# Kernel optimization log

Measured on AMD Instinct MI355X. Metric: run time of the kernel, lower is better.

Reference implementation:

```python
import jax, jax.numpy as jnp
import numpy as np

B, C, Hf, Wf, HM, P = 64, 2048, 16, 16, 256, 10  # P = num_parts, NP = graph nodes
NP = P - 1
EPS = 1e-5  # BatchNorm eps

def bn_eval(x, g, b, rm, rv):
    return (x - rm) * jax.lax.rsqrt(rv + EPS) * g + b

def setup_inputs() -> dict:
    key = jax.random.key(0)
    ks = jax.random.split(key, 6)
    return {
        "x_global": jax.random.normal(ks[0], (B, C, Hf, Wf), jnp.float32),
        "x_gcn": jax.random.normal(ks[1], (B, C, Hf, Wf), jnp.float32),
        "mask": jax.random.randint(ks[2], (B, 1, HM, HM), 0, P, jnp.int32),
        "adj": jax.random.uniform(ks[3], (B, NP, NP), jnp.float32),
        "W1": jax.random.normal(ks[4], (C, C), jnp.float32) * 0.02,
        "b1": jnp.zeros((C,), jnp.float32),
        "g1": jnp.ones((NP * C,), jnp.float32), "be1": jnp.zeros((NP * C,), jnp.float32),
        "rm1": jnp.zeros((NP * C,), jnp.float32), "rv1": jnp.ones((NP * C,), jnp.float32),
        "W2": jax.random.normal(ks[5], (C, C), jnp.float32) * 0.02,
        "b2": jnp.zeros((C,), jnp.float32),
        "g2": jnp.ones((NP * C,), jnp.float32), "be2": jnp.zeros((NP * C,), jnp.float32),
        "rm2": jnp.zeros((NP * C,), jnp.float32), "rv2": jnp.ones((NP * C,), jnp.float32),
        "gb_g": jnp.ones((C,), jnp.float32), "gb_b": jnp.zeros((C,), jnp.float32),
        "gb_rm": jnp.zeros((C,), jnp.float32), "gb_rv": jnp.ones((C,), jnp.float32),
        "gn_g": jnp.ones((C,), jnp.float32), "gn_b": jnp.zeros((C,), jnp.float32),
        "gn_rm": jnp.zeros((C,), jnp.float32), "gn_rv": jnp.ones((C,), jnp.float32),
    }

def gc_layer(x, adj, Wt, bias, g, be, rm, rv):
    # GraphConvolution: matmul -> bmm(adj) -> bias -> BN over flattened (B, NP*C)
    s = jnp.einsum('bpc,cd->bpd', x, Wt)
    o = jnp.einsum('bpq,bqd->bpd', adj, s) + bias
    flat = o.reshape(o.shape[0], -1)
    return bn_eval(flat, g, be, rm, rv).reshape(o.shape)

def reference(x_global, x_gcn, mask, adj, W1, b1, g1, be1, rm1, rv1,
              W2, b2, g2, be2, rm2, rv2, gb_g, gb_b, gb_rm, gb_rv,
              gn_g, gn_b, gn_rm, gn_rv):
    # --- global branch: GAP + bottleneck BN (eval) ---
    feat_global = x_global.mean(axis=(2, 3))                      # (B, C)
    bnfeat_global = bn_eval(feat_global, gb_g, gb_b, gb_rm, gb_rv)

    # --- nearest-neighbor downsample of mask to feature-map size ---
    stride = HM // Hf
    mr = mask[:, 0, ::stride, ::stride]                           # (B, h, w)

    # one-hot part masks for classes 1..P-1: (B, h, w, NP)
    onehot = (mr[..., None] == jnp.arange(1, P)).astype(jnp.float32)
    counts = onehot.sum(axis=(1, 2))                              # (B, NP)

    # deterministic part dropout: drop the first present part per image
    drop = jnp.argmax(counts > 0, axis=1) + 1                     # (B,)
    keep = (mr != drop[:, None, None]).astype(jnp.float32)        # (B, h, w)
    x_self = x_gcn * keep[:, None, :, :]

    # segment mean pooling per part: (B, NP, C)
    denom = (counts + 1e-8)[..., None]
    mask_feat = jnp.einsum('bchw,bhwp->bpc', x_gcn, onehot) / denom
    self_feat = jnp.einsum('bchw,bhwp->bpc', x_self, onehot) / denom

    def gcn(x):
        x1 = jax.nn.relu(gc_layer(x, adj, W1, b1, g1, be1, rm1, rv1))
        x2 = jax.nn.relu(gc_layer(x1, adj, W2, b2, g2, be2, rm2, rv2))
        return x2.mean(axis=1), x2.reshape(x2.shape[0], -1)

    feat_gcn, feat_gcn_cat = gcn(mask_feat)
    feat_self, feat_self_cat = gcn(self_feat)
    bnfeat_gcn = bn_eval(feat_gcn, gn_g, gn_b, gn_rm, gn_rv)
    bnfeat_self = bn_eval(feat_self, gn_g, gn_b, gn_rm, gn_rv)

    # concatenate eval-mode outputs into one array: (B, 3*C + 2*NP*C)
    return jnp.concatenate([bnfeat_global, bnfeat_gcn, bnfeat_self,
                            feat_gcn_cat, feat_self_cat], axis=1)
```

## Files before the change

kernel.cpp:

```cpp
#include <hip/hip_runtime.h>
#include <cstdint>
#include <cstddef>

#define EPSV 1e-5f

typedef __bf16 bf16x8 __attribute__((ext_vector_type(8)));
typedef float f32x4 __attribute__((ext_vector_type(4)));

__device__ __forceinline__ unsigned short f2bf(float f) {
  unsigned int u = __float_as_uint(f);
  u += 0x7FFFu + ((u >> 16) & 1u);
  return (unsigned short)(u >> 16);
}

__device__ __forceinline__ void async_copy16(const void* src, void* dst_lds) {
  __builtin_amdgcn_global_load_lds(
      (const __attribute__((address_space(1))) void*)src,
      (__attribute__((address_space(3))) void*)dst_lds, 16, 0, 0);
}

__global__ __launch_bounds__(256) void prep(
    const float* __restrict__ W1, const float* __restrict__ W2,
    unsigned short* __restrict__ Wt1, unsigned short* __restrict__ Wt2,
    const float* __restrict__ xg, const float* __restrict__ gb_g,
    const float* __restrict__ gb_b, const float* __restrict__ gb_rm,
    const float* __restrict__ gb_rv, float* __restrict__ out,
    const int* __restrict__ mask, int* __restrict__ partid,
    float* __restrict__ invden, int* __restrict__ dropm1,
    const float* __restrict__ b1, const float* __restrict__ g1,
    const float* __restrict__ be1, const float* __restrict__ rm1,
    const float* __restrict__ rv1, const float* __restrict__ b2,
    const float* __restrict__ g2, const float* __restrict__ be2,
    const float* __restrict__ rm2, const float* __restrict__ rv2,
    float* __restrict__ sc1, float* __restrict__ sh1,
    float* __restrict__ sc2, float* __restrict__ sh2) {
  int blk = blockIdx.x;
  if (blk < 8192) {
    int z = blk >> 12;
    int rem = blk & 4095;
    int by = rem >> 6, bx = rem & 63;
    const float* W = z ? W2 : W1;
    unsigned short* Wt = z ? Wt2 : Wt1;
    __shared__ float tile[32][33];
    int tx = threadIdx.x & 31;
    int ty = threadIdx.x >> 5;
    int k0 = by * 32, n0 = bx * 32;
#pragma unroll
    for (int i = 0; i < 32; i += 8)
      tile[ty + i][tx] = W[(size_t)(k0 + ty + i) * 2048 + n0 + tx];
    __syncthreads();
#pragma unroll
    for (int i = 0; i < 32; i += 8)
      Wt[(size_t)(n0 + ty + i) * 2048 + k0 + tx] = f2bf(tile[tx][ty + i]);
  } else if (blk < 16384) {
    int base = (blk - 8192) * 16 + (threadIdx.x >> 6) * 4;
    int lane = threadIdx.x & 63;
    const float4* xp = (const float4*)xg + (size_t)base * 64 + lane;
    float4 v0 = xp[0], v1 = xp[64], v2 = xp[128], v3 = xp[192];
    float s0 = v0.x + v0.y + v0.z + v0.w;
    float s1 = v1.x + v1.y + v1.z + v1.w;
    float s2 = v2.x + v2.y + v2.z + v2.w;
    float s3 = v3.x + v3.y + v3.z + v3.w;
#pragma unroll
    for (int o = 32; o > 0; o >>= 1) {
      s0 += __shfl_xor(s0, o, 64);
      s1 += __shfl_xor(s1, o, 64);
      s2 += __shfl_xor(s2, o, 64);
      s3 += __shfl_xor(s3, o, 64);
    }
    if (lane == 0) {
      int b = base >> 11, c = base & 2047;
      float m[4] = {s0 * (1.f / 256.f), s1 * (1.f / 256.f),
                    s2 * (1.f / 256.f), s3 * (1.f / 256.f)};
      float4 o4;
      float* po = &o4.x;
#pragma unroll
      for (int r = 0; r < 4; r++) {
        int cc = c + r;
        po[r] = (m[r] - gb_rm[cc]) / sqrtf(gb_rv[cc] + EPSV) * gb_g[cc] +
                gb_b[cc];
      }
      *(float4*)(out + (size_t)b * 43008 + c) = o4;
    }
  } else if (blk < 16448) {
    int b = blk - 16384;
    int t = threadIdx.x;
    int h = t >> 4, w = t & 15;
    int m = mask[(size_t)b * 65536 + h * 4096 + w * 16];
    partid[b * 256 + t] = m;
    __shared__ int cnt[10];
    if (t < 10) cnt[t] = 0;
    __syncthreads();
    atomicAdd(&cnt[m], 1);
    __syncthreads();
    if (t == 0) {
      int dp = 0;
      for (int p = 8; p >= 0; p--)
        if (cnt[p + 1] > 0) dp = p;
      dropm1[b] = dp;
    }
    if (t < 9) invden[b * 9 + t] = 1.f / ((float)cnt[t + 1] + 1e-8f);
  } else {
    int i = (blk - 16448) * 256 + threadIdx.x;
    int z = i >= 18432;
    int f = i - z * 18432;
    int d = f & 2047;
    const float* g = z ? g2 : g1;
    const float* be = z ? be2 : be1;
    const float* rm = z ? rm2 : rm1;
    const float* rv = z ? rv2 : rv1;
    const float* bias = z ? b2 : b1;
    float sc = g[f] / sqrtf(rv[f] + EPSV);
    float sh = (bias[d] - rm[f]) * sc + be[f];
    (z ? sc2 : sc1)[f] = sc;
    (z ? sh2 : sh1)[f] = sh;
  }
}

__global__ __launch_bounds__(256) void kpool_mfma(
    const float* __restrict__ x, const int* __restrict__ partid,
    const float* __restrict__ invden, const int* __restrict__ dropm1,
    unsigned short* __restrict__ Abuf) {
  __shared__ unsigned short As[64 * 264];
  __shared__ unsigned short Bs[16 * 264];
  __shared__ int pid[256];
  const int t = threadIdx.x;
  const int b = blockIdx.y;
  const int c0 = blockIdx.x * 64;

  pid[t] = partid[b * 256 + t];

  const float4* xgp = (const float4*)(x + ((size_t)(b * 2048 + c0)) * 256);
#pragma unroll
  for (int it = 0; it < 16; it++) {
    int idx = t + it * 256;
    float4 v = xgp[idx];
    int row = idx >> 6, sc = (idx & 63) * 4;
    ushort4 h;
    h.x = f2bf(v.x); h.y = f2bf(v.y); h.z = f2bf(v.z); h.w = f2bf(v.w);
    *(ushort4*)&As[row * 264 + sc] = h;
  }
  __syncthreads();
  {
    int p = t >> 4, s0 = (t & 15) * 16;
#pragma unroll
    for (int j = 0; j < 16; j++)
      Bs[p * 264 + s0 + j] =
          (pid[s0 + j] == p + 1) ? (unsigned short)0x3F80 : (unsigned short)0;
  }
  __syncthreads();

  const int wave = t >> 6;
  const int l16 = t & 15;
  const int quad = (t & 63) >> 4;
  f32x4 acc = (f32x4){0.f, 0.f, 0.f, 0.f};
#pragma unroll
  for (int ks = 0; ks < 8; ks++) {
    bf16x8 a = *(const bf16x8*)&As[(wave * 16 + l16) * 264 + ks * 32 + quad * 8];
    bf16x8 bf = *(const bf16x8*)&Bs[l16 * 264 + ks * 32 + quad * 8];
    acc = __builtin_amdgcn_mfma_f32_16x16x32_bf16(a, bf, acc, 0, 0, 0);
  }

  if (l16 < 9) {
    int p = l16;
    float inv = invden[b * 9 + p];
    int dm1 = dropm1[b];
    int cbase = c0 + wave * 16 + quad * 4;
    ushort4 hm;
    hm.x = f2bf(acc[0] * inv);
    hm.y = f2bf(acc[1] * inv);
    hm.z = f2bf(acc[2] * inv);
    hm.w = f2bf(acc[3] * inv);
    ushort4 hs = (p == dm1) ? (ushort4){0, 0, 0, 0} : hm;
    *(ushort4*)&Abuf[(size_t)(b * 9 + p) * 2048 + cbase] = hm;
    *(ushort4*)&Abuf[(size_t)((64 + b) * 9 + p) * 2048 + cbase] = hs;
  }
}

#define GK 2048
#define SPART (1152 * 2048)
__global__ __launch_bounds__(256) void gemm_db(
    const unsigned short* __restrict__ A, const unsigned short* __restrict__ Bt,
    float* __restrict__ S) {
  __shared__ unsigned short As[2][128 * 64];
  __shared__ unsigned short Bs[2][64 * 64];
  const int tid = threadIdx.x;
  const int lane = tid & 63;
  const int wave = tid >> 6;
  const int wm = (wave >> 1) << 6;
  const int wn = (wave & 1) << 5;
  const int quad = lane >> 4;
  const int l16 = lane & 15;
  const int by = blockIdx.y;
  const int bx = blockIdx.x;
  const int kz = blockIdx.z;

  const unsigned short* Ag = A + (size_t)by * 128 * GK;
  const unsigned short* Bg = Bt + (size_t)bx * 64 * GK;
  S += (size_t)kz * SPART;

  f32x4 acc[4][2];
#pragma unroll
  for (int i = 0; i < 4; i++)
#pragma unroll
    for (int j = 0; j < 2; j++) acc[i][j] = (f32x4){0.f, 0.f, 0.f, 0.f};

  int srA[4], scA[4];
#pragma unroll
  for (int s = 0; s < 4; s++) {
    int idx = tid + s * 256;
    srA[s] = idx >> 3;
    scA[s] = ((idx & 7) ^ (srA[s] & 7)) * 8;
  }
  int srB[2], scB[2];
#pragma unroll
  for (int s = 0; s < 2; s++) {
    int idx = tid + s * 256;
    srB[s] = idx >> 3;
    scB[s] = ((idx & 7) ^ (srB[s] & 7)) * 8;
  }

  const int kbeg = kz * 1024;

#define STAGE(buf, kk)                                                        \
  do {                                                                        \
    _Pragma("unroll") for (int s = 0; s < 4; s++) {                           \
      int idx = tid + s * 256;                                                \
      async_copy16(Ag + (size_t)srA[s] * GK + (kk) + scA[s],                  \
                   &As[buf][idx * 8]);                                        \
    }                                                                         \
    _Pragma("unroll") for (int s = 0; s < 2; s++) {                           \
      int idx = tid + s * 256;                                                \
      async_copy16(Bg + (size_t)srB[s] * GK + (kk) + scB[s],                  \
                   &Bs[buf][idx * 8]);                                        \
    }                                                                         \
  } while (0)

  STAGE(0, kbeg);
  asm volatile("s_waitcnt vmcnt(0)" ::: "memory");
  __syncthreads();

  for (int it = 0; it < 16; it++) {
    const int cur = it & 1;
    if (it < 15) STAGE(cur ^ 1, kbeg + (it + 1) * 64);

#pragma unroll
    for (int ks = 0; ks < 2; ks++) {
      bf16x8 af[4], bfr[2];
#pragma unroll
      for (int i = 0; i < 4; i++) {
        int row = wm + i * 16 + l16;
        int slot = row * 8 + ((ks * 4 + quad) ^ (row & 7));
        af[i] = *(const bf16x8*)&As[cur][slot * 8];
      }
#pragma unroll
      for (int j = 0; j < 2; j++) {
        int row = wn + j * 16 + l16;
        int slot = row * 8 + ((ks * 4 + quad) ^ (row & 7));
        bfr[j] = *(const bf16x8*)&Bs[cur][slot * 8];
      }
#pragma unroll
      for (int i = 0; i < 4; i++)
#pragma unroll
        for (int j = 0; j < 2; j++)
          acc[i][j] = __builtin_amdgcn_mfma_f32_16x16x32_bf16(
              af[i], bfr[j], acc[i][j], 0, 0, 0);
    }

    if (it < 15) {
      asm volatile("s_waitcnt vmcnt(0)" ::: "memory");
      __syncthreads();
    }
  }

#pragma unroll
  for (int i = 0; i < 4; i++)
#pragma unroll
    for (int j = 0; j < 2; j++)
#pragma unroll
      for (int r = 0; r < 4; r++) {
        int m = by * 128 + wm + i * 16 + quad * 4 + r;
        int n = bx * 64 + wn + j * 16 + l16;
        S[(size_t)m * 2048 + n] = acc[i][j][r];
      }
}

__global__ __launch_bounds__(256) void epi_mid(
    const float* __restrict__ S, const float* __restrict__ adj,
    const float* __restrict__ sc, const float* __restrict__ sh,
    unsigned short* __restrict__ Aout) {
  int idx = blockIdx.x * 256 + threadIdx.x;
  int d = idx & 2047;
  int bb = idx >> 11;
  int b = bb & 63;
  float s[9];
#pragma unroll
  for (int q = 0; q < 9; q++) {
    size_t off = (size_t)(bb * 9 + q) * 2048 + d;
    s[q] = S[off] + S[off + SPART];
  }
#pragma unroll
  for (int p = 0; p < 9; p++) {
    float o = 0.f;
#pragma unroll
    for (int q = 0; q < 9; q++) o += adj[b * 81 + p * 9 + q] * s[q];
    int f = p * 2048 + d;
    float v = fmaxf(o * sc[f] + sh[f], 0.f);
    Aout[(size_t)(bb * 9 + p) * 2048 + d] = f2bf(v);
  }
}

__global__ __launch_bounds__(256) void epi_final(
    const float* __restrict__ S, const float* __restrict__ adj,
    const float* __restrict__ sc, const float* __restrict__ sh,
    const float* __restrict__ gn_g, const float* __restrict__ gn_b,
    const float* __restrict__ gn_rm, const float* __restrict__ gn_rv,
    float* __restrict__ out) {
  int idx = blockIdx.x * 256 + threadIdx.x;
  int d = idx & 2047;
  int bb = idx >> 11;
  int b = bb & 63;
  bool selfb = bb >= 64;
  float s[9];
#pragma unroll
  for (int q = 0; q < 9; q++) {
    size_t off = (size_t)(bb * 9 + q) * 2048 + d;
    s[q] = S[off] + S[off + SPART];
  }
  float* orow = out + (size_t)b * 43008;
  size_t catbase = selfb ? 24576 : 6144;
  float mean = 0.f;
#pragma unroll
  for (int p = 0; p < 9; p++) {
    float o = 0.f;
#pragma unroll
    for (int q = 0; q < 9; q++) o += adj[b * 81 + p * 9 + q] * s[q];
    int f = p * 2048 + d;
    float v = fmaxf(o * sc[f] + sh[f], 0.f);
    mean += v;
    orow[catbase + f] = v;
  }
  mean *= (1.f / 9.f);
  orow[(selfb ? 4096 : 2048) + d] =
      (mean - gn_rm[d]) / sqrtf(gn_rv[d] + EPSV) * gn_g[d] + gn_b[d];
}

extern "C" void kernel_launch(void* const* d_in, const int* in_sizes, int n_in,
                              void* d_out, int out_size, void* d_ws,
                              size_t ws_size, hipStream_t stream) {
  const float* x_global = (const float*)d_in[0];
  const float* x_gcn = (const float*)d_in[1];
  const int* mask = (const int*)d_in[2];
  const float* adj = (const float*)d_in[3];
  const float* W1 = (const float*)d_in[4];
  const float* b1 = (const float*)d_in[5];
  const float* g1 = (const float*)d_in[6];
  const float* be1 = (const float*)d_in[7];
  const float* rm1 = (const float*)d_in[8];
  const float* rv1 = (const float*)d_in[9];
  const float* W2 = (const float*)d_in[10];
  const float* b2 = (const float*)d_in[11];
  const float* g2 = (const float*)d_in[12];
  const float* be2 = (const float*)d_in[13];
  const float* rm2 = (const float*)d_in[14];
  const float* rv2 = (const float*)d_in[15];
  const float* gb_g = (const float*)d_in[16];
  const float* gb_b = (const float*)d_in[17];
  const float* gb_rm = (const float*)d_in[18];
  const float* gb_rv = (const float*)d_in[19];
  const float* gn_g = (const float*)d_in[20];
  const float* gn_b = (const float*)d_in[21];
  const float* gn_rm = (const float*)d_in[22];
  const float* gn_rv = (const float*)d_in[23];
  float* out = (float*)d_out;

  char* ws = (char*)d_ws;
  int* partid = (int*)(ws);
  float* invden = (float*)(ws + 65536);
  int* dropm1 = (int*)(ws + 67840);
  unsigned short* Abuf = (unsigned short*)(ws + 131072);
  unsigned short* Wt1 = (unsigned short*)(ws + 4849664);
  unsigned short* Wt2 = (unsigned short*)(ws + 13238272);
  float* S = (float*)(ws + 21626880);
  float* sc1 = (float*)(ws + 40501248);
  float* sh1 = (float*)(ws + 40574976);
  float* sc2 = (float*)(ws + 40648704);
  float* sh2 = (float*)(ws + 40722432);

  prep<<<16592, 256, 0, stream>>>(W1, W2, Wt1, Wt2, x_global, gb_g, gb_b,
                                  gb_rm, gb_rv, out, mask, partid, invden,
                                  dropm1, b1, g1, be1, rm1, rv1, b2, g2, be2,
                                  rm2, rv2, sc1, sh1, sc2, sh2);
  kpool_mfma<<<dim3(32, 64), 256, 0, stream>>>(x_gcn, partid, invden, dropm1,
                                               Abuf);
  gemm_db<<<dim3(32, 9, 2), 256, 0, stream>>>(Abuf, Wt1, S);
  epi_mid<<<1024, 256, 0, stream>>>(S, adj, sc1, sh1, Abuf);
  gemm_db<<<dim3(32, 9, 2), 256, 0, stream>>>(Abuf, Wt2, S);
  epi_final<<<1024, 256, 0, stream>>>(S, adj, sc2, sh2, gn_g, gn_b, gn_rm,
                                      gn_rv, out);
}
```

Measured before the change: 407.3 us.

## Apply adjacency before the weight GEMMs and fuse BN/ReLU into GEMM epilogue

Uses associativity (adj·(X·W) = (adj·X)·W) to mix the pooled features with the adjacency before each GEMM, so the BN-scale/shift and ReLU epilogue can be fused directly into the GEMM output. This removes the fp32 split-K S buffer and its two full read/write passes, and derives the self-branch mix by subtracting the dropped part's contribution. GEMM tiles shrink to 64x64 without split-K to keep enough blocks, and a small premix kernel plus a mean/BN kernel replace the old epilogues. Intermediate mixed activations are rounded to bf16 at different points than before, which changes numerics slightly.

```diff
diff --git a/kernel.cpp b/kernel.cpp
--- a/kernel.cpp
+++ b/kernel.cpp
@@ -3,6 +3,7 @@
 #include <cstddef>
 
 #define EPSV 1e-5f
+#define GK 2048
 
 typedef __bf16 bf16x8 __attribute__((ext_vector_type(8)));
 typedef float f32x4 __attribute__((ext_vector_type(4)));
@@ -11,6 +12,10 @@
   unsigned int u = __float_as_uint(f);
   u += 0x7FFFu + ((u >> 16) & 1u);
   return (unsigned short)(u >> 16);
+}
+
+__device__ __forceinline__ float bf2f(unsigned short h) {
+  return __uint_as_float((unsigned int)h << 16);
 }
 
 __device__ __forceinline__ void async_copy16(const void* src, void* dst_lds) {
@@ -117,18 +122,21 @@
   }
 }
 
-__global__ __launch_bounds__(256) void kpool_mfma(
+__global__ __launch_bounds__(256) void kpool_mix(
     const float* __restrict__ x, const int* __restrict__ partid,
     const float* __restrict__ invden, const int* __restrict__ dropm1,
-    unsigned short* __restrict__ Abuf) {
+    const float* __restrict__ adj, unsigned short* __restrict__ Amix) {
   __shared__ unsigned short As[64 * 264];
   __shared__ unsigned short Bs[16 * 264];
   __shared__ int pid[256];
+  __shared__ float pools[9][64];
+  __shared__ float adjs[81];
   const int t = threadIdx.x;
   const int b = blockIdx.y;
   const int c0 = blockIdx.x * 64;
 
   pid[t] = partid[b * 256 + t];
+  if (t < 81) adjs[t] = adj[b * 81 + t];
 
   const float4* xgp = (const float4*)(x + ((size_t)(b * 2048 + c0)) * 256);
 #pragma unroll
@@ -162,93 +170,89 @@
   }
 
   if (l16 < 9) {
-    int p = l16;
-    float inv = invden[b * 9 + p];
-    int dm1 = dropm1[b];
-    int cbase = c0 + wave * 16 + quad * 4;
-    ushort4 hm;
-    hm.x = f2bf(acc[0] * inv);
-    hm.y = f2bf(acc[1] * inv);
-    hm.z = f2bf(acc[2] * inv);
-    hm.w = f2bf(acc[3] * inv);
-    ushort4 hs = (p == dm1) ? (ushort4){0, 0, 0, 0} : hm;
-    *(ushort4*)&Abuf[(size_t)(b * 9 + p) * 2048 + cbase] = hm;
-    *(ushort4*)&Abuf[(size_t)((64 + b) * 9 + p) * 2048 + cbase] = hs;
-  }
-}
-
-#define GK 2048
-#define SPART (1152 * 2048)
-__global__ __launch_bounds__(256) void gemm_db(
+    float inv = invden[b * 9 + l16];
+    int cb = wave * 16 + quad * 4;
+#pragma unroll
+    for (int r = 0; r < 4; r++) pools[l16][cb + r] = acc[r] * inv;
+  }
+  __syncthreads();
+
+  const int dm1 = dropm1[b];
+  const int col = t & 63;
+  const int pp = t >> 6;
+  const float pd = pools[dm1][col];
+#pragma unroll
+  for (int p = pp; p < 9; p += 4) {
+    float m = 0.f;
+#pragma unroll
+    for (int q = 0; q < 9; q++) m += adjs[p * 9 + q] * pools[q][col];
+    float sf = m - adjs[p * 9 + dm1] * pd;
+    Amix[(size_t)(b * 9 + p) * 2048 + c0 + col] = f2bf(m);
+    Amix[(size_t)((64 + b) * 9 + p) * 2048 + c0 + col] = f2bf(sf);
+  }
+}
+
+template <int MODE>
+__global__ __launch_bounds__(256) void gemm_fused(
     const unsigned short* __restrict__ A, const unsigned short* __restrict__ Bt,
-    float* __restrict__ S) {
-  __shared__ unsigned short As[2][128 * 64];
+    const float* __restrict__ sc, const float* __restrict__ sh,
+    void* __restrict__ dstv) {
+  __shared__ unsigned short As[2][64 * 64];
   __shared__ unsigned short Bs[2][64 * 64];
   const int tid = threadIdx.x;
   const int lane = tid & 63;
   const int wave = tid >> 6;
-  const int wm = (wave >> 1) << 6;
+  const int wm = (wave >> 1) << 5;
   const int wn = (wave & 1) << 5;
   const int quad = lane >> 4;
   const int l16 = lane & 15;
   const int by = blockIdx.y;
   const int bx = blockIdx.x;
-  const int kz = blockIdx.z;
-
-  const unsigned short* Ag = A + (size_t)by * 128 * GK;
+
+  const unsigned short* Ag = A + (size_t)by * 64 * GK;
   const unsigned short* Bg = Bt + (size_t)bx * 64 * GK;
-  S += (size_t)kz * SPART;
-
-  f32x4 acc[4][2];
-#pragma unroll
-  for (int i = 0; i < 4; i++)
+
+  f32x4 acc[2][2];
+#pragma unroll
+  for (int i = 0; i < 2; i++)
 #pragma unroll
     for (int j = 0; j < 2; j++) acc[i][j] = (f32x4){0.f, 0.f, 0.f, 0.f};
 
-  int srA[4], scA[4];
-#pragma unroll
-  for (int s = 0; s < 4; s++) {
-    int idx = tid + s * 256;
-    srA[s] = idx >> 3;
-    scA[s] = ((idx & 7) ^ (srA[s] & 7)) * 8;
-  }
-  int srB[2], scB[2];
+  int sr[2], scx[2];
 #pragma unroll
   for (int s = 0; s < 2; s++) {
     int idx = tid + s * 256;
-    srB[s] = idx >> 3;
-    scB[s] = ((idx & 7) ^ (srB[s] & 7)) * 8;
-  }
-
-  const int kbeg = kz * 1024;
+    sr[s] = idx >> 3;
+    scx[s] = ((idx & 7) ^ (sr[s] & 7)) * 8;
+  }
 
 #define STAGE(buf, kk)                                                        \
   do {                                                                        \
-    _Pragma("unroll") for (int s = 0; s < 4; s++) {                           \
+    _Pragma("unroll") for (int s = 0; s < 2; s++) {                           \
       int idx = tid + s * 256;                                                \
-      async_copy16(Ag + (size_t)srA[s] * GK + (kk) + scA[s],                  \
+      async_copy16(Ag + (size_t)sr[s] * GK + (kk) + scx[s],                   \
                    &As[buf][idx * 8]);                                        \
     }                                                                         \
     _Pragma("unroll") for (int s = 0; s < 2; s++) {                           \
       int idx = tid + s * 256;                                                \
-      async_copy16(Bg + (size_t)srB[s] * GK + (kk) + scB[s],                  \
+      async_copy16(Bg + (size_t)sr[s] * GK + (kk) + scx[s],                   \
                    &Bs[buf][idx * 8]);                                        \
     }                                                                         \
   } while (0)
 
-  STAGE(0, kbeg);
+  STAGE(0, 0);
   asm volatile("s_waitcnt vmcnt(0)" ::: "memory");
   __syncthreads();
 
-  for (int it = 0; it < 16; it++) {
+  for (int it = 0; it < 32; it++) {
     const int cur = it & 1;
-    if (it < 15) STAGE(cur ^ 1, kbeg + (it + 1) * 64);
+    if (it < 31) STAGE(cur ^ 1, (it + 1) * 64);
 
 #pragma unroll
     for (int ks = 0; ks < 2; ks++) {
-      bf16x8 af[4], bfr[2];
-#pragma unroll
-      for (int i = 0; i < 4; i++) {
+      bf16x8 af[2], bfr[2];
+#pragma unroll
+      for (int i = 0; i < 2; i++) {
         int row = wm + i * 16 + l16;
         int slot = row * 8 + ((ks * 4 + quad) ^ (row & 7));
         af[i] = *(const bf16x8*)&As[cur][slot * 8];
@@ -260,59 +264,74 @@
         bfr[j] = *(const bf16x8*)&Bs[cur][slot * 8];
       }
 #pragma unroll
-      for (int i = 0; i < 4; i++)
+      for (int i = 0; i < 2; i++)
 #pragma unroll
         for (int j = 0; j < 2; j++)
           acc[i][j] = __builtin_amdgcn_mfma_f32_16x16x32_bf16(
               af[i], bfr[j], acc[i][j], 0, 0, 0);
     }
 
-    if (it < 15) {
+    if (it < 31) {
       asm volatile("s_waitcnt vmcnt(0)" ::: "memory");
       __syncthreads();
     }
   }
-
-#pragma unroll
-  for (int i = 0; i < 4; i++)
+#undef STAGE
+
+#pragma unroll
+  for (int i = 0; i < 2; i++)
 #pragma unroll
     for (int j = 0; j < 2; j++)
 #pragma unroll
       for (int r = 0; r < 4; r++) {
-        int m = by * 128 + wm + i * 16 + quad * 4 + r;
+        int m = by * 64 + wm + i * 16 + quad * 4 + r;
         int n = bx * 64 + wn + j * 16 + l16;
-        S[(size_t)m * 2048 + n] = acc[i][j][r];
+        int bb = m / 9;
+        int p = m - bb * 9;
+        int f = p * 2048 + n;
+        float v = fmaxf(acc[i][j][r] * sc[f] + sh[f], 0.f);
+        if (MODE == 0) {
+          ((unsigned short*)dstv)[(size_t)m * 2048 + n] = f2bf(v);
+        } else {
+          int b = bb & 63;
+          size_t base = (size_t)b * 43008 + (bb >= 64 ? 24576 : 6144);
+          ((float*)dstv)[base + f] = v;
+        }
       }
 }
 
-__global__ __launch_bounds__(256) void epi_mid(
-    const float* __restrict__ S, const float* __restrict__ adj,
-    const float* __restrict__ sc, const float* __restrict__ sh,
-    unsigned short* __restrict__ Aout) {
-  int idx = blockIdx.x * 256 + threadIdx.x;
-  int d = idx & 2047;
-  int bb = idx >> 11;
-  int b = bb & 63;
-  float s[9];
+__global__ __launch_bounds__(256) void premix2(
+    const unsigned short* __restrict__ A2, const float* __restrict__ adj,
+    unsigned short* __restrict__ Amix) {
+  __shared__ float adjs[81];
+  const int bb = blockIdx.y;
+  const int b = bb & 63;
+  const int t = threadIdx.x;
+  if (t < 81) adjs[t] = adj[b * 81 + t];
+  __syncthreads();
+  const int col = blockIdx.x * 512 + t * 2;
+  float q0[9], q1[9];
 #pragma unroll
   for (int q = 0; q < 9; q++) {
-    size_t off = (size_t)(bb * 9 + q) * 2048 + d;
-    s[q] = S[off] + S[off + SPART];
+    unsigned int u = *(const unsigned int*)&A2[(size_t)(bb * 9 + q) * 2048 + col];
+    q0[q] = bf2f((unsigned short)(u & 0xFFFF));
+    q1[q] = bf2f((unsigned short)(u >> 16));
   }
 #pragma unroll
   for (int p = 0; p < 9; p++) {
-    float o = 0.f;
-#pragma unroll
-    for (int q = 0; q < 9; q++) o += adj[b * 81 + p * 9 + q] * s[q];
-    int f = p * 2048 + d;
-    float v = fmaxf(o * sc[f] + sh[f], 0.f);
-    Aout[(size_t)(bb * 9 + p) * 2048 + d] = f2bf(v);
-  }
-}
-
-__global__ __launch_bounds__(256) void epi_final(
-    const float* __restrict__ S, const float* __restrict__ adj,
-    const float* __restrict__ sc, const float* __restrict__ sh,
+    float a0 = 0.f, a1 = 0.f;
+#pragma unroll
+    for (int q = 0; q < 9; q++) {
+      float w = adjs[p * 9 + q];
+      a0 += w * q0[q];
+      a1 += w * q1[q];
+    }
+    unsigned int o = (unsigned int)f2bf(a0) | ((unsigned int)f2bf(a1) << 16);
+    *(unsigned int*)&Amix[(size_t)(bb * 9 + p) * 2048 + col] = o;
+  }
+}
+
+__global__ __launch_bounds__(256) void meanbn(
     const float* __restrict__ gn_g, const float* __restrict__ gn_b,
     const float* __restrict__ gn_rm, const float* __restrict__ gn_rv,
     float* __restrict__ out) {
@@ -321,27 +340,12 @@
   int bb = idx >> 11;
   int b = bb & 63;
   bool selfb = bb >= 64;
-  float s[9];
-#pragma unroll
-  for (int q = 0; q < 9; q++) {
-    size_t off = (size_t)(bb * 9 + q) * 2048 + d;
-    s[q] = S[off] + S[off + SPART];
-  }
-  float* orow = out + (size_t)b * 43008;
-  size_t catbase = selfb ? 24576 : 6144;
-  float mean = 0.f;
-#pragma unroll
-  for (int p = 0; p < 9; p++) {
-    float o = 0.f;
-#pragma unroll
-    for (int q = 0; q < 9; q++) o += adj[b * 81 + p * 9 + q] * s[q];
-    int f = p * 2048 + d;
-    float v = fmaxf(o * sc[f] + sh[f], 0.f);
-    mean += v;
-    orow[catbase + f] = v;
-  }
-  mean *= (1.f / 9.f);
-  orow[(selfb ? 4096 : 2048) + d] =
+  const float* orow = out + (size_t)b * 43008 + (selfb ? 24576 : 6144);
+  float s = 0.f;
+#pragma unroll
+  for (int p = 0; p < 9; p++) s += orow[p * 2048 + d];
+  float mean = s * (1.f / 9.f);
+  out[(size_t)b * 43008 + (selfb ? 4096 : 2048) + d] =
       (mean - gn_rm[d]) / sqrtf(gn_rv[d] + EPSV) * gn_g[d] + gn_b[d];
 }
 
@@ -378,24 +382,23 @@
   int* partid = (int*)(ws);
   float* invden = (float*)(ws + 65536);
   int* dropm1 = (int*)(ws + 67840);
-  unsigned short* Abuf = (unsigned short*)(ws + 131072);
-  unsigned short* Wt1 = (unsigned short*)(ws + 4849664);
-  unsigned short* Wt2 = (unsigned short*)(ws + 13238272);
-  float* S = (float*)(ws + 21626880);
-  float* sc1 = (float*)(ws + 40501248);
-  float* sh1 = (float*)(ws + 40574976);
-  float* sc2 = (float*)(ws + 40648704);
-  float* sh2 = (float*)(ws + 40722432);
+  unsigned short* Amix = (unsigned short*)(ws + 131072);
+  unsigned short* A2 = (unsigned short*)(ws + 4849664);
+  unsigned short* Wt1 = (unsigned short*)(ws + 9568256);
+  unsigned short* Wt2 = (unsigned short*)(ws + 17956864);
+  float* sc1 = (float*)(ws + 26345472);
+  float* sh1 = (float*)(ws + 26419200);
+  float* sc2 = (float*)(ws + 26492928);
+  float* sh2 = (float*)(ws + 26566656);
 
   prep<<<16592, 256, 0, stream>>>(W1, W2, Wt1, Wt2, x_global, gb_g, gb_b,
                                   gb_rm, gb_rv, out, mask, partid, invden,
                                   dropm1, b1, g1, be1, rm1, rv1, b2, g2, be2,
                                   rm2, rv2, sc1, sh1, sc2, sh2);
-  kpool_mfma<<<dim3(32, 64), 256, 0, stream>>>(x_gcn, partid, invden, dropm1,
-                                               Abuf);
-  gemm_db<<<dim3(32, 9, 2), 256, 0, stream>>>(Abuf, Wt1, S);
-  epi_mid<<<1024, 256, 0, stream>>>(S, adj, sc1, sh1, Abuf);
-  gemm_db<<<dim3(32, 9, 2), 256, 0, stream>>>(Abuf, Wt2, S);
-  epi_final<<<1024, 256, 0, stream>>>(S, adj, sc2, sh2, gn_g, gn_b, gn_rm,
-                                      gn_rv, out);
-}
+  kpool_mix<<<dim3(32, 64), 256, 0, stream>>>(x_gcn, partid, invden, dropm1,
+                                              adj, Amix);
+  gemm_fused<0><<<dim3(32, 18), 256, 0, stream>>>(Amix, Wt1, sc1, sh1, A2);
+  premix2<<<dim3(4, 128), 256, 0, stream>>>(A2, adj, Amix);
+  gemm_fused<1><<<dim3(32, 18), 256, 0, stream>>>(Amix, Wt2, sc2, sh2, out);
+  meanbn<<<1024, 256, 0, stream>>>(gn_g, gn_b, gn_rm, gn_rv, out);
+}
```

After: 419.3 us. 1.03x slower.
